# Optimization experiments

Hardware: AMD Instinct MI355X
Metric: run time of the kernel (lower is better)

Reference implementation:

```python
import jax, jax.numpy as jnp
import numpy as np

B, N = 2048, 64
D, H = 64, 256
CARD_V, UNIT_V, ENEMY_V, AT_V, SRC_V, MODE_V, TER_V, SITE_V, SKILL_V = 400, 100, 120, 50, 30, 10, 12, 25, 60
STATE_SC, CE_SC, SITE_SC, ME_SC, ACT_SC = 64, 8, 6, 8, 16
L_HAND, L_UNIT, L_CE, L_SK, L_VS, L_ME, L_TGT = 16, 8, 8, 8, 16, 16, 8
STATE_IN = STATE_SC + 6 * D + (D + CE_SC) + (D + SITE_SC) + (D + ME_SC)  # 662
ACT_IN = 7 * D + ACT_SC  # 464


def setup_inputs() -> dict:
    key = jax.random.key(0)
    ks = iter(jax.random.split(key, 64))
    nrm = lambda shape, s=1.0: jax.random.normal(next(ks), shape, jnp.float32) * s
    ri = lambda shape, hi: jax.random.randint(next(ks), shape, 0, hi, jnp.int32)
    return {
        'state_scalars': nrm((B, STATE_SC)),
        'mode_id': ri((B,), MODE_V), 'terrain_id': ri((B,), TER_V), 'site_type_id': ri((B,), SITE_V),
        'hand_ids': ri((B, L_HAND), CARD_V), 'hand_mask': ri((B, L_HAND), 2),
        'unit_ids': ri((B, L_UNIT), UNIT_V), 'unit_mask': ri((B, L_UNIT), 2),
        'combat_enemy_ids': ri((B, L_CE), ENEMY_V), 'combat_enemy_scalars': nrm((B, L_CE, CE_SC)), 'combat_enemy_mask': ri((B, L_CE), 2),
        'skill_ids': ri((B, L_SK), SKILL_V), 'skill_mask': ri((B, L_SK), 2),
        'visible_site_ids': ri((B, L_VS), SITE_V), 'visible_site_scalars': nrm((B, L_VS, SITE_SC)), 'visible_site_mask': ri((B, L_VS), 2),
        'map_enemy_ids': ri((B, L_ME), ENEMY_V), 'map_enemy_scalars': nrm((B, L_ME, ME_SC)), 'map_enemy_mask': ri((B, L_ME), 2),
        'action_ids': ri((B, N, 6), SRC_V),  # SRC_V=30 is min over the 6 id vocabs -> always in range
        'action_scalars': nrm((B, N, ACT_SC)),
        'target_enemy_ids': ri((B, N, L_TGT), ENEMY_V), 'target_mask': ri((B, N, L_TGT), 2),
        'card_emb': nrm((CARD_V, D), 0.05), 'unit_emb': nrm((UNIT_V, D), 0.05), 'enemy_emb': nrm((ENEMY_V, D), 0.05),
        'action_type_emb': nrm((AT_V, D), 0.05), 'source_emb': nrm((SRC_V, D), 0.05), 'mode_emb': nrm((MODE_V, D), 0.05),
        'terrain_emb': nrm((TER_V, D), 0.05), 'site_emb': nrm((SITE_V, D), 0.05), 'skill_emb': nrm((SKILL_V, D), 0.05),
        'map_site_emb': nrm((SITE_V, D), 0.05),
        'W_s': nrm((STATE_IN, H), 0.02), 'b_s': jnp.zeros((H,), jnp.float32),
        'W_a': nrm((ACT_IN, H), 0.02), 'b_a': jnp.zeros((H,), jnp.float32),
        'W1': nrm((2 * H, H), 0.02), 'b1': jnp.zeros((H,), jnp.float32),
        'W2': nrm((H, 1), 0.02), 'b2': jnp.zeros((1,), jnp.float32),
        'W_v': nrm((H, 1), 0.02), 'b_v': jnp.zeros((1,), jnp.float32),
    }


def masked_mean(x, mask):
    # x: [..., L, D'], mask: [..., L] (0/1). Empty list -> zeros (count clamped to 1).
    m = mask.astype(x.dtype)[..., None]
    s = jnp.sum(x * m, axis=-2)
    c = jnp.maximum(jnp.sum(m, axis=-2), 1.0)
    return s / c


def reference(state_scalars, mode_id, terrain_id, site_type_id, hand_ids, hand_mask,
              unit_ids, unit_mask, combat_enemy_ids, combat_enemy_scalars, combat_enemy_mask,
              skill_ids, skill_mask, visible_site_ids, visible_site_scalars, visible_site_mask,
              map_enemy_ids, map_enemy_scalars, map_enemy_mask, action_ids, action_scalars,
              target_enemy_ids, target_mask, card_emb, unit_emb, enemy_emb, action_type_emb,
              source_emb, mode_emb, terrain_emb, site_emb, skill_emb, map_site_emb,
              W_s, b_s, W_a, b_a, W1, b1, W2, b2, W_v, b_v):
    # ---- state encoding (batched version of encode_state) ----
    hand_pool = masked_mean(card_emb[hand_ids], hand_mask)            # [B, D]
    unit_pool = masked_mean(unit_emb[unit_ids], unit_mask)            # [B, D]
    ce = jnp.concatenate([enemy_emb[combat_enemy_ids], combat_enemy_scalars], axis=-1)
    ce_pool = masked_mean(ce, combat_enemy_mask)                      # [B, D+CE_SC]
    skill_pool = masked_mean(skill_emb[skill_ids], skill_mask)        # [B, D]
    vs = jnp.concatenate([map_site_emb[visible_site_ids], visible_site_scalars], axis=-1)
    vs_pool = masked_mean(vs, visible_site_mask)                      # [B, D+SITE_SC]
    me = jnp.concatenate([enemy_emb[map_enemy_ids], map_enemy_scalars], axis=-1)
    me_pool = masked_mean(me, map_enemy_mask)                         # [B, D+ME_SC]
    state_input = jnp.concatenate([
        state_scalars, mode_emb[mode_id], hand_pool, unit_pool,
        terrain_emb[terrain_id], site_emb[site_type_id],
        ce_pool, skill_pool, vs_pool, me_pool], axis=-1)              # [B, 662]
    state_repr = jnp.tanh(state_input @ W_s + b_s)                    # [B, H]
    # ---- action encoding (batched encode_actions) ----
    tgt_pool = masked_mean(enemy_emb[target_enemy_ids], target_mask)  # [B, N, D]
    action_input = jnp.concatenate([
        action_type_emb[action_ids[..., 0]], source_emb[action_ids[..., 1]],
        card_emb[action_ids[..., 2]], unit_emb[action_ids[..., 3]],
        enemy_emb[action_ids[..., 4]], skill_emb[action_ids[..., 5]],
        tgt_pool, action_scalars], axis=-1)                           # [B, N, 464]
    action_reprs = jnp.tanh(action_input @ W_a + b_a)                 # [B, N, H]
    # ---- scoring + value heads ----
    state_b = jnp.broadcast_to(state_repr[:, None, :], (state_repr.shape[0], action_reprs.shape[1], state_repr.shape[1]))
    combined = jnp.concatenate([state_b, action_reprs], axis=-1)      # [B, N, 2H]
    logits = (jnp.tanh(combined @ W1 + b1) @ W2 + b2)[..., 0]         # [B, N]
    value = (state_repr @ W_v + b_v)[..., 0]                          # [B]
    return logits, value
```

## Files before the change

### kernel.cpp

```cpp
#include <hip/hip_runtime.h>
#include <hip/hip_bf16.h>

#define BB 2048
#define NN 64
#define DD 64
#define HH 256
#define L_HAND 16
#define L_UNIT 8
#define L_CE 8
#define L_SK 8
#define L_VS 16
#define L_ME 16
#define L_TGT 8
#define STATE_SC 64
#define CE_SC 8
#define SITE_SC 6
#define ME_SC 8
#define ACT_SC 16
#define STATE_IN 662
#define ACT_IN 464

#define SROWS 4
#define SK 672
#define SSTRIDE 676

typedef __attribute__((ext_vector_type(8))) short short8;
typedef __attribute__((ext_vector_type(4))) float f32x4;

__device__ __forceinline__ float fast_tanh(float x) {
    float e = __expf(2.0f * x);
    return 1.0f - 2.0f / (e + 1.0f);
}
__device__ __forceinline__ short f2bs(float x) {
    __hip_bfloat16 h = __float2bfloat16(x);
    return *reinterpret_cast<short*>(&h);
}
__device__ __forceinline__ float bs2f(short u) {
    union { unsigned int i; float f; } v;
    v.i = ((unsigned int)(unsigned short)u) << 16;
    return v.f;
}

#define RO_AT    0
#define RO_SRC   50
#define RO_CARD  80
#define RO_UNIT  480
#define RO_ENEMY 580
#define RO_SKILL 700
#define EMB_ROWS 760

#define T0 (480 * 256)
#define T1 (T0 + 256 * 256)
#define T2 (T1 + EMB_ROWS * 64)
#define T3 (T2 + SK * 256)
#define T4 (T3 + 256 * 256)

__global__ __launch_bounds__(256) void pack_kernel(
    const float* __restrict__ W_a, const float* __restrict__ W1,
    const float* __restrict__ W_s,
    const float* __restrict__ at_emb, const float* __restrict__ src_emb,
    const float* __restrict__ card_emb, const float* __restrict__ unit_emb,
    const float* __restrict__ enemy_emb, const float* __restrict__ skill_emb,
    ushort* __restrict__ WaP, ushort* __restrict__ W1bP, ushort* __restrict__ emb16,
    ushort* __restrict__ WsP, ushort* __restrict__ W1aP)
{
    const int idx = blockIdx.x * 256 + threadIdx.x;
    if (idx < T0) {
        const int k = idx >> 8, n = idx & 255;
        const float v = (k < ACT_IN) ? W_a[k * HH + n] : 0.f;
        const int pi = (((k >> 5) * 16 + (n >> 4)) * 64 +
                        ((n & 15) + 16 * ((k >> 3) & 3))) * 8 + (k & 7);
        WaP[pi] = (ushort)f2bs(v);
    } else if (idx < T1) {
        const int j = idx - T0;
        const int k = j >> 8, n = j & 255;
        const float v = W1[(256 + k) * HH + n];
        const int pi = (((k >> 5) * 16 + (n >> 4)) * 64 +
                        ((n & 15) + 16 * ((k >> 3) & 3))) * 8 + (k & 7);
        W1bP[pi] = (ushort)f2bs(v);
    } else if (idx < T2) {
        const int j = idx - T1;
        const int row = j >> 6, d = j & 63;
        float v;
        if      (row < RO_SRC)   v = at_emb[row * 64 + d];
        else if (row < RO_CARD)  v = src_emb[(row - RO_SRC) * 64 + d];
        else if (row < RO_UNIT)  v = card_emb[(row - RO_CARD) * 64 + d];
        else if (row < RO_ENEMY) v = unit_emb[(row - RO_UNIT) * 64 + d];
        else if (row < RO_SKILL) v = enemy_emb[(row - RO_ENEMY) * 64 + d];
        else                     v = skill_emb[(row - RO_SKILL) * 64 + d];
        emb16[j] = (ushort)f2bs(v);
    } else if (idx < T3) {
        const int j = idx - T2;
        const int k = j >> 8, n = j & 255;
        const float v = (k < STATE_IN) ? W_s[k * HH + n] : 0.f;
        const int pi = (((k >> 5) * 16 + (n >> 4)) * 64 +
                        ((n & 15) + 16 * ((k >> 3) & 3))) * 8 + (k & 7);
        WsP[pi] = (ushort)f2bs(v);
    } else if (idx < T4) {
        const int j = idx - T3;
        const int k = j >> 8, n = j & 255;
        const float v = W1[k * HH + n];
        const int pi = (((k >> 5) * 16 + (n >> 4)) * 64 +
                        ((n & 15) + 16 * ((k >> 3) & 3))) * 8 + (k & 7);
        W1aP[pi] = (ushort)f2bs(v);
    }
}

__global__ __launch_bounds__(256) void state_mfma_kernel(
    const float* __restrict__ state_scalars,
    const int* __restrict__ mode_id, const int* __restrict__ terrain_id,
    const int* __restrict__ site_type_id,
    const int* __restrict__ hand_ids, const int* __restrict__ hand_mask,
    const int* __restrict__ unit_ids, const int* __restrict__ unit_mask,
    const int* __restrict__ ce_ids, const float* __restrict__ ce_sc, const int* __restrict__ ce_mask,
    const int* __restrict__ skill_ids, const int* __restrict__ skill_mask,
    const int* __restrict__ vs_ids, const float* __restrict__ vs_sc, const int* __restrict__ vs_mask,
    const int* __restrict__ me_ids, const float* __restrict__ me_sc, const int* __restrict__ me_mask,
    const float* __restrict__ mode_emb, const float* __restrict__ ter_emb,
    const float* __restrict__ site_emb, const float* __restrict__ msite_emb,
    const ushort* __restrict__ emb16,
    const ushort* __restrict__ WsP, const float* __restrict__ b_s,
    const ushort* __restrict__ W1aP,
    const float* __restrict__ W_v, const float* __restrict__ b_v,
    float* __restrict__ s_part, float* __restrict__ out_value)
{
    __shared__ float s_in[SROWS * SSTRIDE];
    __shared__ ushort sA2[8 * 64 * 8];
    __shared__ float red[4][4];

    const int t = threadIdx.x;
    const int b0 = blockIdx.x * SROWS;
    const int w = t >> 6;
    const int lane = t & 63;
    const ushort* card16  = emb16 + RO_CARD  * 64;
    const ushort* unit16  = emb16 + RO_UNIT  * 64;
    const ushort* enemy16 = emb16 + RO_ENEMY * 64;
    const ushort* skill16 = emb16 + RO_SKILL * 64;

    for (int u = t; u < SROWS * 84; u += 256) {
        const int r  = u / 84;
        const int un = u - r * 84;
        const int b  = b0 + r;
        float* dst = s_in + r * SSTRIDE;
        if (un < 8) {
            const int o0 = un * 8;
            const float4 f0 = *(const float4*)(state_scalars + b * STATE_SC + o0);
            const float4 f1 = *(const float4*)(state_scalars + b * STATE_SC + o0 + 4);
            *(float4*)(dst + o0) = f0; *(float4*)(dst + o0 + 4) = f1;
        } else if (un < 16) {
            const int d0 = (un - 8) * 8;
            const float4 f0 = *(const float4*)(mode_emb + mode_id[b] * DD + d0);
            const float4 f1 = *(const float4*)(mode_emb + mode_id[b] * DD + d0 + 4);
            *(float4*)(dst + 64 + d0) = f0; *(float4*)(dst + 64 + d0 + 4) = f1;
        } else if (un < 24) {
            const int d0 = (un - 16) * 8;
            float acc[8] = {0,0,0,0,0,0,0,0}; int c = 0;
#pragma unroll
            for (int l = 0; l < L_HAND; ++l) {
                const int mk = hand_mask[b * L_HAND + l]; c += mk;
                const float fm = (float)mk;
                const short8 e = *(const short8*)(card16 + hand_ids[b * L_HAND + l] * 64 + d0);
#pragma unroll
                for (int q = 0; q < 8; ++q) acc[q] = fmaf(fm, bs2f(e[q]), acc[q]);
            }
            const float inv = 1.0f / (float)(c > 1 ? c : 1);
#pragma unroll
            for (int q = 0; q < 8; ++q) dst[128 + d0 + q] = acc[q] * inv;
        } else if (un < 32) {
            const int d0 = (un - 24) * 8;
            float acc[8] = {0,0,0,0,0,0,0,0}; int c = 0;
#pragma unroll
            for (int l = 0; l < L_UNIT; ++l) {
                const int mk = unit_mask[b * L_UNIT + l]; c += mk;
                const float fm = (float)mk;
                const short8 e = *(const short8*)(unit16 + unit_ids[b * L_UNIT + l] * 64 + d0);
#pragma unroll
                for (int q = 0; q < 8; ++q) acc[q] = fmaf(fm, bs2f(e[q]), acc[q]);
            }
            const float inv = 1.0f / (float)(c > 1 ? c : 1);
#pragma unroll
            for (int q = 0; q < 8; ++q) dst[192 + d0 + q] = acc[q] * inv;
        } else if (un < 40) {
            const int d0 = (un - 32) * 8;
            const float4 f0 = *(const float4*)(ter_emb + terrain_id[b] * DD + d0);
            const float4 f1 = *(const float4*)(ter_emb + terrain_id[b] * DD + d0 + 4);
            *(float4*)(dst + 256 + d0) = f0; *(float4*)(dst + 256 + d0 + 4) = f1;
        } else if (un < 48) {
            const int d0 = (un - 40) * 8;
            const float4 f0 = *(const float4*)(site_emb + site_type_id[b] * DD + d0);
            const float4 f1 = *(const float4*)(site_emb + site_type_id[b] * DD + d0 + 4);
            *(float4*)(dst + 320 + d0) = f0; *(float4*)(dst + 320 + d0 + 4) = f1;
        } else if (un < 56) {
            const int d0 = (un - 48) * 8;
            float acc[8] = {0,0,0,0,0,0,0,0}; int c = 0;
#pragma unroll
            for (int l = 0; l < L_CE; ++l) {
                const int mk = ce_mask[b * L_CE + l]; c += mk;
                const float fm = (float)mk;
                const short8 e = *(const short8*)(enemy16 + ce_ids[b * L_CE + l] * 64 + d0);
#pragma unroll
                for (int q = 0; q < 8; ++q) acc[q] = fmaf(fm, bs2f(e[q]), acc[q]);
            }
            const float inv = 1.0f / (float)(c > 1 ? c : 1);
#pragma unroll
            for (int q = 0; q < 8; ++q) dst[384 + d0 + q] = acc[q] * inv;
        } else if (un == 56) {
            float acc[8] = {0,0,0,0,0,0,0,0}; int c = 0;
#pragma unroll
            for (int l = 0; l < L_CE; ++l) {
                const int mk = ce_mask[b * L_CE + l]; c += mk;
                const float fm = (float)mk;
                const float4 f0 = *(const float4*)(ce_sc + (b * L_CE + l) * CE_SC);
                const float4 f1 = *(const float4*)(ce_sc + (b * L_CE + l) * CE_SC + 4);
                acc[0] = fmaf(fm, f0.x, acc[0]); acc[1] = fmaf(fm, f0.y, acc[1]);
                acc[2] = fmaf(fm, f0.z, acc[2]); acc[3] = fmaf(fm, f0.w, acc[3]);
                acc[4] = fmaf(fm, f1.x, acc[4]); acc[5] = fmaf(fm, f1.y, acc[5]);
                acc[6] = fmaf(fm, f1.z, acc[6]); acc[7] = fmaf(fm, f1.w, acc[7]);
            }
            const float inv = 1.0f / (float)(c > 1 ? c : 1);
#pragma unroll
            for (int q = 0; q < 8; ++q) dst[448 + q] = acc[q] * inv;
        } else if (un < 65) {
            const int d0 = (un - 57) * 8;
            float acc[8] = {0,0,0,0,0,0,0,0}; int c = 0;
#pragma unroll
            for (int l = 0; l < L_SK; ++l) {
                const int mk = skill_mask[b * L_SK + l]; c += mk;
                const float fm = (float)mk;
                const short8 e = *(const short8*)(skill16 + skill_ids[b * L_SK + l] * 64 + d0);
#pragma unroll
                for (int q = 0; q < 8; ++q) acc[q] = fmaf(fm, bs2f(e[q]), acc[q]);
            }
            const float inv = 1.0f / (float)(c > 1 ? c : 1);
#pragma unroll
            for (int q = 0; q < 8; ++q) dst[456 + d0 + q] = acc[q] * inv;
        } else if (un < 73) {
            const int d0 = (un - 65) * 8;
            float acc[8] = {0,0,0,0,0,0,0,0}; int c = 0;
#pragma unroll
            for (int l = 0; l < L_VS; ++l) {
                const int mk = vs_mask[b * L_VS + l]; c += mk;
                const float fm = (float)mk;
                const float4 f0 = *(const float4*)(msite_emb + vs_ids[b * L_VS + l] * DD + d0);
                const float4 f1 = *(const float4*)(msite_emb + vs_ids[b * L_VS + l] * DD + d0 + 4);
                acc[0] = fmaf(fm, f0.x, acc[0]); acc[1] = fmaf(fm, f0.y, acc[1]);
                acc[2] = fmaf(fm, f0.z, acc[2]); acc[3] = fmaf(fm, f0.w, acc[3]);
                acc[4] = fmaf(fm, f1.x, acc[4]); acc[5] = fmaf(fm, f1.y, acc[5]);
                acc[6] = fmaf(fm, f1.z, acc[6]); acc[7] = fmaf(fm, f1.w, acc[7]);
            }
            const float inv = 1.0f / (float)(c > 1 ? c : 1);
#pragma unroll
            for (int q = 0; q < 8; ++q) dst[520 + d0 + q] = acc[q] * inv;
        } else if (un == 73) {
            float acc[6] = {0,0,0,0,0,0}; int c = 0;
#pragma unroll
            for (int l = 0; l < L_VS; ++l) {
                const int mk = vs_mask[b * L_VS + l]; c += mk;
                const float fm = (float)mk;
                const float* p = vs_sc + (b * L_VS + l) * SITE_SC;
#pragma unroll
                for (int q = 0; q < 6; ++q) acc[q] = fmaf(fm, p[q], acc[q]);
            }
            const float inv = 1.0f / (float)(c > 1 ? c : 1);
#pragma unroll
            for (int q = 0; q < 6; ++q) dst[584 + q] = acc[q] * inv;
        } else if (un < 82) {
            const int d0 = (un - 74) * 8;
            float acc[8] = {0,0,0,0,0,0,0,0}; int c = 0;
#pragma unroll
            for (int l = 0; l < L_ME; ++l) {
                const int mk = me_mask[b * L_ME + l]; c += mk;
                const float fm = (float)mk;
                const short8 e = *(const short8*)(enemy16 + me_ids[b * L_ME + l] * 64 + d0);
#pragma unroll
                for (int q = 0; q < 8; ++q) acc[q] = fmaf(fm, bs2f(e[q]), acc[q]);
            }
            const float inv = 1.0f / (float)(c > 1 ? c : 1);
#pragma unroll
            for (int q = 0; q < 8; ++q) dst[590 + d0 + q] = acc[q] * inv;
        } else if (un == 82) {
            float acc[8] = {0,0,0,0,0,0,0,0}; int c = 0;
#pragma unroll
            for (int l = 0; l < L_ME; ++l) {
                const int mk = me_mask[b * L_ME + l]; c += mk;
                const float fm = (float)mk;
                const float4 f0 = *(const float4*)(me_sc + (b * L_ME + l) * ME_SC);
                const float4 f1 = *(const float4*)(me_sc + (b * L_ME + l) * ME_SC + 4);
                acc[0] = fmaf(fm, f0.x, acc[0]); acc[1] = fmaf(fm, f0.y, acc[1]);
                acc[2] = fmaf(fm, f0.z, acc[2]); acc[3] = fmaf(fm, f0.w, acc[3]);
                acc[4] = fmaf(fm, f1.x, acc[4]); acc[5] = fmaf(fm, f1.y, acc[5]);
                acc[6] = fmaf(fm, f1.z, acc[6]); acc[7] = fmaf(fm, f1.w, acc[7]);
            }
            const float inv = 1.0f / (float)(c > 1 ? c : 1);
#pragma unroll
            for (int q = 0; q < 8; ++q) dst[654 + q] = acc[q] * inv;
        } else {
#pragma unroll
            for (int q = 0; q < 10; ++q) dst[662 + q] = 0.f;
        }
    }
    __syncthreads();

    const short8* Ws8  = (const short8*)WsP;
    const short8* W1a8 = (const short8*)W1aP;
    const f32x4 zero = {0.f, 0.f, 0.f, 0.f};
    const int m15 = lane & 15;
    const int g = lane >> 4;
    const float* arow = s_in + (m15 & 3) * SSTRIDE;

    f32x4 acc1[4];
#pragma unroll
    for (int nt = 0; nt < 4; ++nt) acc1[nt] = zero;

    for (int kt = 0; kt < 21; ++kt) {
        const int k0 = kt * 32 + 8 * g;
        const float4 v0 = *(const float4*)(arow + k0);
        const float4 v1 = *(const float4*)(arow + k0 + 4);
        short8 a;
        a[0] = f2bs(v0.x); a[1] = f2bs(v0.y); a[2] = f2bs(v0.z); a[3] = f2bs(v0.w);
        a[4] = f2bs(v1.x); a[5] = f2bs(v1.y); a[6] = f2bs(v1.z); a[7] = f2bs(v1.w);
        short8 bfr[4];
#pragma unroll
        for (int nt = 0; nt < 4; ++nt) bfr[nt] = Ws8[(kt * 16 + w * 4 + nt) * 64 + lane];
#pragma unroll
        for (int nt = 0; nt < 4; ++nt)
            acc1[nt] = __builtin_amdgcn_mfma_f32_16x16x32_bf16(a, bfr[nt], acc1[nt], 0, 0, 0);
    }

    float sr[4][4];
    float pv[4] = {0.f, 0.f, 0.f, 0.f};
#pragma unroll
    for (int nt = 0; nt < 4; ++nt) {
        const int n = w * 64 + nt * 16 + m15;
        const float bsn = b_s[n];
        const float wvn = W_v[n];
#pragma unroll
        for (int r = 0; r < 4; ++r) {
            const float sv = fast_tanh(acc1[nt][r] + bsn);
            sr[nt][r] = sv;
            pv[r] = fmaf(sv, wvn, pv[r]);
        }
    }
#pragma unroll
    for (int r = 0; r < 4; ++r) {
        float v = pv[r];
        v += __shfl_xor(v, 1);
        v += __shfl_xor(v, 2);
        v += __shfl_xor(v, 4);
        v += __shfl_xor(v, 8);
        if (lane == 0) red[w][r] = v;
    }
    if (g == 0) {
#pragma unroll
        for (int nt = 0; nt < 4; ++nt) {
            const int n = w * 64 + nt * 16 + m15;
            const int kt2 = n >> 5;
            const int lo16 = (n >> 3) & 3;
#pragma unroll
            for (int r = 0; r < 4; ++r) {
                const int pi = (kt2 * 64 + (r + 16 * lo16)) * 8 + (n & 7);
                sA2[pi] = (ushort)f2bs(sr[nt][r]);
            }
        }
    }
    __syncthreads();

    if (t < SROWS) {
        out_value[b0 + t] = red[0][t] + red[1][t] + red[2][t] + red[3][t] + b_v[0];
    }

    const short8* sA2_8 = (const short8*)sA2;
    f32x4 acc2[4];
#pragma unroll
    for (int nt = 0; nt < 4; ++nt) acc2[nt] = zero;
#pragma unroll
    for (int kt = 0; kt < 8; ++kt) {
        const short8 a2 = sA2_8[kt * 64 + lane];
        short8 bfr[4];
#pragma unroll
        for (int nt = 0; nt < 4; ++nt) bfr[nt] = W1a8[(kt * 16 + w * 4 + nt) * 64 + lane];
#pragma unroll
        for (int nt = 0; nt < 4; ++nt)
            acc2[nt] = __builtin_amdgcn_mfma_f32_16x16x32_bf16(a2, bfr[nt], acc2[nt], 0, 0, 0);
    }
    if (g == 0) {
#pragma unroll
        for (int nt = 0; nt < 4; ++nt) {
            const int n = w * 64 + nt * 16 + m15;
#pragma unroll
            for (int r = 0; r < 4; ++r)
                s_part[(b0 + r) * HH + n] = acc2[nt][r];
        }
    }
}

__device__ __forceinline__ short8 build_chunk(
    int kc, int m, int b,
    const int* __restrict__ s_ids, const int* __restrict__ s_tid,
    const int* __restrict__ s_tmk, const ushort* __restrict__ emb16,
    const float* __restrict__ action_scalars)
{
    const int k0 = kc << 3;
    short8 val;
    if (k0 < 384) {
        const int j = k0 >> 6;
        int roff;
        if      (j == 0) roff = RO_AT;
        else if (j == 1) roff = RO_SRC;
        else if (j == 2) roff = RO_CARD;
        else if (j == 3) roff = RO_UNIT;
        else if (j == 4) roff = RO_ENEMY;
        else             roff = RO_SKILL;
        const int id = s_ids[m * 6 + j];
        val = *(const short8*)(emb16 + (roff + id) * 64 + (k0 & 63));
    } else if (k0 < 448) {
        const int d = k0 - 384;
        const ushort* enemy16 = emb16 + RO_ENEMY * 64;
        float accq[8] = {0.f, 0.f, 0.f, 0.f, 0.f, 0.f, 0.f, 0.f};
        int c = 0;
#pragma unroll
        for (int l = 0; l < L_TGT; ++l) {
            const int mk = s_tmk[m * 8 + l];
            c += mk;
            const float fm = (float)mk;
            const short8 e = *(const short8*)(enemy16 + s_tid[m * 8 + l] * 64 + d);
#pragma unroll
            for (int q = 0; q < 8; ++q) accq[q] = fmaf(fm, bs2f(e[q]), accq[q]);
        }
        const float inv = 1.0f / (float)(c > 1 ? c : 1);
#pragma unroll
        for (int q = 0; q < 8; ++q) val[q] = f2bs(accq[q] * inv);
    } else if (k0 < 464) {
        const float* sc = action_scalars + (b * NN + m) * ACT_SC + (k0 - 448);
        const float4 f0 = *(const float4*)sc;
        const float4 f1 = *(const float4*)(sc + 4);
        val[0] = f2bs(f0.x); val[1] = f2bs(f0.y); val[2] = f2bs(f0.z); val[3] = f2bs(f0.w);
        val[4] = f2bs(f1.x); val[5] = f2bs(f1.y); val[6] = f2bs(f1.z); val[7] = f2bs(f1.w);
    } else {
#pragma unroll
        for (int q = 0; q < 8; ++q) val[q] = 0;
    }
    return val;
}

__global__ __launch_bounds__(512) void action_mfma_kernel(
    const int* __restrict__ action_ids, const float* __restrict__ action_scalars,
    const int* __restrict__ tgt_ids, const int* __restrict__ tgt_mask,
    const ushort* __restrict__ emb16,
    const ushort* __restrict__ WaP, const float* __restrict__ b_a,
    const ushort* __restrict__ W1bP, const float* __restrict__ b1,
    const float* __restrict__ W2, const float* __restrict__ b2,
    const float* __restrict__ s_part, float* __restrict__ out_logits)
{
    __shared__ ushort sA[8 * 4 * 64 * 8];
    __shared__ float red[8][64];
    __shared__ int s_ids[64 * 6];
    __shared__ int s_tid[64 * 8];
    __shared__ int s_tmk[64 * 8];

    const int t = threadIdx.x;
    const int b = blockIdx.x;
    const int w = t >> 6;
    const int lane = t & 63;

    for (int i = t; i < 64 * 6; i += 512) s_ids[i] = action_ids[b * (64 * 6) + i];
    for (int i = t; i < 64 * 8; i += 512) {
        s_tid[i] = tgt_ids[b * (64 * 8) + i];
        s_tmk[i] = tgt_mask[b * (64 * 8) + i];
    }
    __syncthreads();

    const short8* sA8  = (const short8*)sA;
    short8* sA8w = (short8*)sA;
    const short8* Wa8  = (const short8*)WaP;
    const short8* W1b8 = (const short8*)W1bP;
    const f32x4 zero = {0.f, 0.f, 0.f, 0.f};
    const int m15 = lane & 15;
    const int m = lane;
    const int mt_b = m >> 4, mrow = m & 15;

    for (int kc = w; kc < 32; kc += 8) {
        const short8 val = build_chunk(kc, m, b, s_ids, s_tid, s_tmk, emb16, action_scalars);
        const int kt = kc >> 2, lo = kc & 3;
        sA8w[(kt * 4 + mt_b) * 64 + mrow + 16 * lo] = val;
    }
    __syncthreads();

    float ba[2];
#pragma unroll
    for (int nt = 0; nt < 2; ++nt) ba[nt] = b_a[w * 32 + nt * 16 + m15];

    f32x4 acc[4][2];
#pragma unroll
    for (int i = 0; i < 4; ++i) { acc[i][0] = zero; acc[i][1] = zero; }

    short8 bn0 = Wa8[(w * 2 + 0) * 64 + lane];
    short8 bn1 = Wa8[(w * 2 + 1) * 64 + lane];
#pragma unroll
    for (int kt = 0; kt < 8; ++kt) {
        const short8 b0 = bn0, b1 = bn1;
        bn0 = Wa8[((kt + 1) * 16 + w * 2 + 0) * 64 + lane];
        bn1 = Wa8[((kt + 1) * 16 + w * 2 + 1) * 64 + lane];
        short8 a[4];
#pragma unroll
        for (int mti = 0; mti < 4; ++mti) a[mti] = sA8[(kt * 4 + mti) * 64 + lane];
#pragma unroll
        for (int mti = 0; mti < 4; ++mti) {
            acc[mti][0] = __builtin_amdgcn_mfma_f32_16x16x32_bf16(a[mti], b0, acc[mti][0], 0, 0, 0);
            acc[mti][1] = __builtin_amdgcn_mfma_f32_16x16x32_bf16(a[mti], b1, acc[mti][1], 0, 0, 0);
        }
    }
    __syncthreads();

    for (int kc = 32 + w; kc < 60; kc += 8) {
        const short8 val = build_chunk(kc, m, b, s_ids, s_tid, s_tmk, emb16, action_scalars);
        const int ktl = (kc >> 2) - 8, lo = kc & 3;
        sA8w[(ktl * 4 + mt_b) * 64 + mrow + 16 * lo] = val;
    }
    __syncthreads();

#pragma unroll
    for (int kt = 8; kt < 15; ++kt) {
        const short8 b0 = bn0, b1 = bn1;
        if (kt < 14) {
            bn0 = Wa8[((kt + 1) * 16 + w * 2 + 0) * 64 + lane];
            bn1 = Wa8[((kt + 1) * 16 + w * 2 + 1) * 64 + lane];
        }
        short8 a[4];
#pragma unroll
        for (int mti = 0; mti < 4; ++mti) a[mti] = sA8[((kt - 8) * 4 + mti) * 64 + lane];
#pragma unroll
        for (int mti = 0; mti < 4; ++mti) {
            acc[mti][0] = __builtin_amdgcn_mfma_f32_16x16x32_bf16(a[mti], b0, acc[mti][0], 0, 0, 0);
            acc[mti][1] = __builtin_amdgcn_mfma_f32_16x16x32_bf16(a[mti], b1, acc[mti][1], 0, 0, 0);
        }
    }
    __syncthreads();

    short8 cn0 = W1b8[(w * 2 + 0) * 64 + lane];
    short8 cn1 = W1b8[(w * 2 + 1) * 64 + lane];

#pragma unroll
    for (int mti = 0; mti < 4; ++mti)
#pragma unroll
        for (int nt = 0; nt < 2; ++nt) {
            const int n = w * 32 + nt * 16 + m15;
            const int kt2 = n >> 5;
            const int lo16 = (n >> 3) & 3;
#pragma unroll
            for (int r = 0; r < 4; ++r) {
                const int mm = mti * 16 + (lane >> 4) * 4 + r;
                const float h = fast_tanh(acc[mti][nt][r] + ba[nt]);
                const int pi = ((kt2 * 4 + mti) * 64 + ((mm & 15) + 16 * lo16)) * 8 + (n & 7);
                sA[pi] = (ushort)f2bs(h);
            }
        }
    __syncthreads();

    float sp[2], w2v[2];
#pragma unroll
    for (int nt = 0; nt < 2; ++nt) {
        const int n = w * 32 + nt * 16 + m15;
        sp[nt]  = s_part[b * HH + n] + b1[n];
        w2v[nt] = W2[n];
    }

#pragma unroll
    for (int i = 0; i < 4; ++i) { acc[i][0] = zero; acc[i][1] = zero; }

#pragma unroll
    for (int kt = 0; kt < 8; ++kt) {
        const short8 b0 = cn0, b1 = cn1;
        if (kt < 7) {
            cn0 = W1b8[((kt + 1) * 16 + w * 2 + 0) * 64 + lane];
            cn1 = W1b8[((kt + 1) * 16 + w * 2 + 1) * 64 + lane];
        }
        short8 a[4];
#pragma unroll
        for (int mti = 0; mti < 4; ++mti) a[mti] = sA8[(kt * 4 + mti) * 64 + lane];
#pragma unroll
        for (int mti = 0; mti < 4; ++mti) {
            acc[mti][0] = __builtin_amdgcn_mfma_f32_16x16x32_bf16(a[mti], b0, acc[mti][0], 0, 0, 0);
            acc[mti][1] = __builtin_amdgcn_mfma_f32_16x16x32_bf16(a[mti], b1, acc[mti][1], 0, 0, 0);
        }
    }

    float part[4][4];
#pragma unroll
    for (int mti = 0; mti < 4; ++mti)
#pragma unroll
        for (int r = 0; r < 4; ++r) part[mti][r] = 0.f;

#pragma unroll
    for (int mti = 0; mti < 4; ++mti)
#pragma unroll
        for (int nt = 0; nt < 2; ++nt)
#pragma unroll
            for (int r = 0; r < 4; ++r)
                part[mti][r] += fast_tanh(acc[mti][nt][r] + sp[nt]) * w2v[nt];

#pragma unroll
    for (int mti = 0; mti < 4; ++mti)
#pragma unroll
        for (int r = 0; r < 4; ++r) {
            float v = part[mti][r];
            v += __shfl_xor(v, 1);
            v += __shfl_xor(v, 2);
            v += __shfl_xor(v, 4);
            v += __shfl_xor(v, 8);
            part[mti][r] = v;
        }
    if (m15 == 0) {
#pragma unroll
        for (int mti = 0; mti < 4; ++mti)
#pragma unroll
            for (int r = 0; r < 4; ++r) {
                const int mm = mti * 16 + (lane >> 4) * 4 + r;
                red[w][mm] = part[mti][r];
            }
    }
    __syncthreads();
    if (t < 64) {
        float s = b2[0];
#pragma unroll
        for (int wi = 0; wi < 8; ++wi) s += red[wi][t];
        out_logits[b * NN + t] = s;
    }
}

extern "C" void kernel_launch(void* const* d_in, const int* in_sizes, int n_in,
                              void* d_out, int out_size, void* d_ws, size_t ws_size,
                              hipStream_t stream) {
    const float* state_scalars = (const float*)d_in[0];
    const int*   mode_id       = (const int*)d_in[1];
    const int*   terrain_id    = (const int*)d_in[2];
    const int*   site_type_id  = (const int*)d_in[3];
    const int*   hand_ids      = (const int*)d_in[4];
    const int*   hand_mask     = (const int*)d_in[5];
    const int*   unit_ids      = (const int*)d_in[6];
    const int*   unit_mask     = (const int*)d_in[7];
    const int*   ce_ids        = (const int*)d_in[8];
    const float* ce_sc         = (const float*)d_in[9];
    const int*   ce_mask       = (const int*)d_in[10];
    const int*   skill_ids     = (const int*)d_in[11];
    const int*   skill_mask    = (const int*)d_in[12];
    const int*   vs_ids        = (const int*)d_in[13];
    const float* vs_sc         = (const float*)d_in[14];
    const int*   vs_mask       = (const int*)d_in[15];
    const int*   me_ids        = (const int*)d_in[16];
    const float* me_sc         = (const float*)d_in[17];
    const int*   me_mask       = (const int*)d_in[18];
    const int*   action_ids    = (const int*)d_in[19];
    const float* action_scalars= (const float*)d_in[20];
    const int*   tgt_ids       = (const int*)d_in[21];
    const int*   tgt_mask      = (const int*)d_in[22];
    const float* card_emb      = (const float*)d_in[23];
    const float* unit_emb      = (const float*)d_in[24];
    const float* enemy_emb     = (const float*)d_in[25];
    const float* at_emb        = (const float*)d_in[26];
    const float* src_emb       = (const float*)d_in[27];
    const float* mode_emb      = (const float*)d_in[28];
    const float* ter_emb       = (const float*)d_in[29];
    const float* site_emb      = (const float*)d_in[30];
    const float* skill_emb     = (const float*)d_in[31];
    const float* msite_emb     = (const float*)d_in[32];
    const float* W_s           = (const float*)d_in[33];
    const float* b_s           = (const float*)d_in[34];
    const float* W_a           = (const float*)d_in[35];
    const float* b_a           = (const float*)d_in[36];
    const float* W1            = (const float*)d_in[37];
    const float* b1            = (const float*)d_in[38];
    const float* W2            = (const float*)d_in[39];
    const float* b2            = (const float*)d_in[40];
    const float* W_v           = (const float*)d_in[41];
    const float* b_v           = (const float*)d_in[42];

    float* out_logits = (float*)d_out;
    float* out_value  = (float*)d_out + (size_t)BB * NN;

    char* ws = (char*)d_ws;
    float*  s_part = (float*)ws;
    ushort* WaP    = (ushort*)(ws + 2097152);
    ushort* W1bP   = (ushort*)(ws + 2342912);
    ushort* emb16  = (ushort*)(ws + 2473984);
    ushort* WsP    = (ushort*)(ws + 2571264);
    ushort* W1aP   = (ushort*)(ws + 2915328);

    pack_kernel<<<(T4 + 255) / 256, 256, 0, stream>>>(
        W_a, W1, W_s, at_emb, src_emb, card_emb, unit_emb, enemy_emb, skill_emb,
        WaP, W1bP, emb16, WsP, W1aP);

    state_mfma_kernel<<<BB / SROWS, 256, 0, stream>>>(
        state_scalars, mode_id, terrain_id, site_type_id,
        hand_ids, hand_mask, unit_ids, unit_mask,
        ce_ids, ce_sc, ce_mask, skill_ids, skill_mask,
        vs_ids, vs_sc, vs_mask, me_ids, me_sc, me_mask,
        mode_emb, ter_emb, site_emb, msite_emb, emb16,
        WsP, b_s, W1aP, W_v, b_v, s_part, out_value);

    action_mfma_kernel<<<BB, 512, 0, stream>>>(
        action_ids, action_scalars, tgt_ids, tgt_mask,
        emb16, WaP, b_a, W1bP, b1, W2, b2, s_part, out_logits);
}
```

Baseline: 123.7 us.

## Stream embedding gathers into LDS asynchronously and reorder action GEMM k-tiles

Embedding-row gathers for the action input now go straight from global memory into LDS via global_load_lds. The tail (target pooling and scalars) is built first, and the GEMM k-loop is reordered (0-7, then 12-14, then 8-11) so the second batch of async gathers overlaps with MFMA work. The change also swaps the tanh division for a hardware reciprocal and replaces the shuffle-xor reduction with DPP row shifts. The aim is to hide gather latency and cut register round trips. The trade-offs are a larger LDS footprint, and correctness now relies on async-copy completion ordering at the barriers.

```diff
diff --git a/kernel.cpp b/kernel.cpp
--- a/kernel.cpp
+++ b/kernel.cpp
@@ -29,7 +29,7 @@
 
 __device__ __forceinline__ float fast_tanh(float x) {
     float e = __expf(2.0f * x);
-    return 1.0f - 2.0f / (e + 1.0f);
+    return 1.0f - 2.0f * __builtin_amdgcn_rcpf(e + 1.0f);
 }
 __device__ __forceinline__ short f2bs(float x) {
     __hip_bfloat16 h = __float2bfloat16(x);
@@ -39,6 +39,23 @@
     union { unsigned int i; float f; } v;
     v.i = ((unsigned int)(unsigned short)u) << 16;
     return v.f;
+}
+__device__ __forceinline__ void async_copy16(const void* gsrc, void* ldst) {
+    __builtin_amdgcn_global_load_lds(
+        (const __attribute__((address_space(1))) unsigned int*)gsrc,
+        (__attribute__((address_space(3))) unsigned int*)ldst, 16, 0, 0);
+}
+__device__ __forceinline__ float sum16_dpp(float v) {
+    int x;
+    x = __builtin_amdgcn_update_dpp(0, __float_as_int(v), 0x111, 0xf, 0xf, true);
+    v += __int_as_float(x);
+    x = __builtin_amdgcn_update_dpp(0, __float_as_int(v), 0x112, 0xf, 0xf, true);
+    v += __int_as_float(x);
+    x = __builtin_amdgcn_update_dpp(0, __float_as_int(v), 0x114, 0xf, 0xf, true);
+    v += __int_as_float(x);
+    x = __builtin_amdgcn_update_dpp(0, __float_as_int(v), 0x118, 0xf, 0xf, true);
+    v += __int_as_float(x);
+    return v;
 }
 
 #define RO_AT    0
@@ -394,26 +411,13 @@
     }
 }
 
-__device__ __forceinline__ short8 build_chunk(
-    int kc, int m, int b,
-    const int* __restrict__ s_ids, const int* __restrict__ s_tid,
-    const int* __restrict__ s_tmk, const ushort* __restrict__ emb16,
-    const float* __restrict__ action_scalars)
+__device__ __forceinline__ short8 tail_chunk(
+    int k0, int m, int b,
+    const int* __restrict__ s_tid, const int* __restrict__ s_tmk,
+    const ushort* __restrict__ emb16, const float* __restrict__ action_scalars)
 {
-    const int k0 = kc << 3;
     short8 val;
-    if (k0 < 384) {
-        const int j = k0 >> 6;
-        int roff;
-        if      (j == 0) roff = RO_AT;
-        else if (j == 1) roff = RO_SRC;
-        else if (j == 2) roff = RO_CARD;
-        else if (j == 3) roff = RO_UNIT;
-        else if (j == 4) roff = RO_ENEMY;
-        else             roff = RO_SKILL;
-        const int id = s_ids[m * 6 + j];
-        val = *(const short8*)(emb16 + (roff + id) * 64 + (k0 & 63));
-    } else if (k0 < 448) {
+    if (k0 < 448) {
         const int d = k0 - 384;
         const ushort* enemy16 = emb16 + RO_ENEMY * 64;
         float accq[8] = {0.f, 0.f, 0.f, 0.f, 0.f, 0.f, 0.f, 0.f};
@@ -452,7 +456,7 @@
     const float* __restrict__ W2, const float* __restrict__ b2,
     const float* __restrict__ s_part, float* __restrict__ out_logits)
 {
-    __shared__ ushort sA[8 * 4 * 64 * 8];
+    __shared__ ushort sA[11 * 2048];
     __shared__ float red[8][64];
     __shared__ int s_ids[64 * 6];
     __shared__ int s_tid[64 * 8];
@@ -462,45 +466,66 @@
     const int b = blockIdx.x;
     const int w = t >> 6;
     const int lane = t & 63;
-
-    for (int i = t; i < 64 * 6; i += 512) s_ids[i] = action_ids[b * (64 * 6) + i];
-    for (int i = t; i < 64 * 8; i += 512) {
-        s_tid[i] = tgt_ids[b * (64 * 8) + i];
-        s_tmk[i] = tgt_mask[b * (64 * 8) + i];
-    }
-    __syncthreads();
+    const int m15 = lane & 15;
 
     const short8* sA8  = (const short8*)sA;
     short8* sA8w = (short8*)sA;
     const short8* Wa8  = (const short8*)WaP;
     const short8* W1b8 = (const short8*)W1bP;
     const f32x4 zero = {0.f, 0.f, 0.f, 0.f};
-    const int m15 = lane & 15;
-    const int m = lane;
-    const int mt_b = m >> 4, mrow = m & 15;
-
-    for (int kc = w; kc < 32; kc += 8) {
-        const short8 val = build_chunk(kc, m, b, s_ids, s_tid, s_tmk, emb16, action_scalars);
-        const int kt = kc >> 2, lo = kc & 3;
-        sA8w[(kt * 4 + mt_b) * 64 + mrow + 16 * lo] = val;
-    }
-    __syncthreads();
-
-    float ba[2];
-#pragma unroll
-    for (int nt = 0; nt < 2; ++nt) ba[nt] = b_a[w * 32 + nt * 16 + m15];
-
-    f32x4 acc[4][2];
-#pragma unroll
-    for (int i = 0; i < 4; ++i) { acc[i][0] = zero; acc[i][1] = zero; }
 
     short8 bn0 = Wa8[(w * 2 + 0) * 64 + lane];
     short8 bn1 = Wa8[(w * 2 + 1) * 64 + lane];
+
+    for (int i = t; i < 64 * 6; i += 512) s_ids[i] = action_ids[b * (64 * 6) + i];
+    for (int i = t; i < 64 * 8; i += 512) {
+        s_tid[i] = tgt_ids[b * (64 * 8) + i];
+        s_tmk[i] = tgt_mask[b * (64 * 8) + i];
+    }
+    __syncthreads();
+
+    const int ROFFS[6] = {RO_AT, RO_SRC, RO_CARD, RO_UNIT, RO_ENEMY, RO_SKILL};
+
+    {
+        const int kt = w;
+        const int j = kt >> 1;
+        const int roff = ROFFS[j];
+        const int koff = (kt & 1) * 32 + (lane >> 4) * 8;
+#pragma unroll
+        for (int i = 0; i < 4; ++i) {
+            const int id = s_ids[(i * 16 + m15) * 6 + j];
+            const ushort* src = emb16 + (roff + id) * 64 + koff;
+            async_copy16(src, sA + kt * 2048 + i * 512);
+        }
+    }
+
+    {
+        const int m = lane;
+        const int mt_b = m >> 4, mrow = m & 15;
+        for (int kc = 48 + w; kc < 60; kc += 8) {
+            const int k0 = kc << 3;
+            const short8 val = tail_chunk(k0, m, b, s_tid, s_tmk, emb16, action_scalars);
+            const int ktl = (k0 >> 5) - 4;
+            const int lo = kc & 3;
+            sA8w[(ktl * 4 + mt_b) * 64 + mrow + 16 * lo] = val;
+        }
+    }
+    __syncthreads();
+
+    float ba[2];
+#pragma unroll
+    for (int nt = 0; nt < 2; ++nt) ba[nt] = b_a[w * 32 + nt * 16 + m15];
+
+    f32x4 acc[4][2];
+#pragma unroll
+    for (int i = 0; i < 4; ++i) { acc[i][0] = zero; acc[i][1] = zero; }
+
 #pragma unroll
     for (int kt = 0; kt < 8; ++kt) {
         const short8 b0 = bn0, b1 = bn1;
-        bn0 = Wa8[((kt + 1) * 16 + w * 2 + 0) * 64 + lane];
-        bn1 = Wa8[((kt + 1) * 16 + w * 2 + 1) * 64 + lane];
+        const int nkt = (kt < 7) ? kt + 1 : 12;
+        bn0 = Wa8[(nkt * 16 + w * 2 + 0) * 64 + lane];
+        bn1 = Wa8[(nkt * 16 + w * 2 + 1) * 64 + lane];
         short8 a[4];
 #pragma unroll
         for (int mti = 0; mti < 4; ++mti) a[mti] = sA8[(kt * 4 + mti) * 64 + lane];
@@ -512,23 +537,28 @@
     }
     __syncthreads();
 
-    for (int kc = 32 + w; kc < 60; kc += 8) {
-        const short8 val = build_chunk(kc, m, b, s_ids, s_tid, s_tmk, emb16, action_scalars);
-        const int ktl = (kc >> 2) - 8, lo = kc & 3;
-        sA8w[(ktl * 4 + mt_b) * 64 + mrow + 16 * lo] = val;
-    }
-    __syncthreads();
-
-#pragma unroll
-    for (int kt = 8; kt < 15; ++kt) {
+    if (w < 4) {
+        const int kt = 8 + w;
+        const int j = kt >> 1;
+        const int roff = ROFFS[j];
+        const int koff = (kt & 1) * 32 + (lane >> 4) * 8;
+#pragma unroll
+        for (int i = 0; i < 4; ++i) {
+            const int id = s_ids[(i * 16 + m15) * 6 + j];
+            const ushort* src = emb16 + (roff + id) * 64 + koff;
+            async_copy16(src, sA + (kt - 8) * 2048 + i * 512);
+        }
+    }
+
+#pragma unroll
+    for (int kt = 12; kt < 15; ++kt) {
         const short8 b0 = bn0, b1 = bn1;
-        if (kt < 14) {
-            bn0 = Wa8[((kt + 1) * 16 + w * 2 + 0) * 64 + lane];
-            bn1 = Wa8[((kt + 1) * 16 + w * 2 + 1) * 64 + lane];
-        }
+        const int nkt = (kt < 14) ? kt + 1 : 8;
+        bn0 = Wa8[(nkt * 16 + w * 2 + 0) * 64 + lane];
+        bn1 = Wa8[(nkt * 16 + w * 2 + 1) * 64 + lane];
         short8 a[4];
 #pragma unroll
-        for (int mti = 0; mti < 4; ++mti) a[mti] = sA8[((kt - 8) * 4 + mti) * 64 + lane];
+        for (int mti = 0; mti < 4; ++mti) a[mti] = sA8[((kt - 4) * 4 + mti) * 64 + lane];
 #pragma unroll
         for (int mti = 0; mti < 4; ++mti) {
             acc[mti][0] = __builtin_amdgcn_mfma_f32_16x16x32_bf16(a[mti], b0, acc[mti][0], 0, 0, 0);
@@ -537,8 +567,27 @@
     }
     __syncthreads();
 
-    short8 cn0 = W1b8[(w * 2 + 0) * 64 + lane];
-    short8 cn1 = W1b8[(w * 2 + 1) * 64 + lane];
+    short8 cn0, cn1;
+#pragma unroll
+    for (int kt = 8; kt < 12; ++kt) {
+        const short8 b0 = bn0, b1 = bn1;
+        if (kt < 11) {
+            bn0 = Wa8[((kt + 1) * 16 + w * 2 + 0) * 64 + lane];
+            bn1 = Wa8[((kt + 1) * 16 + w * 2 + 1) * 64 + lane];
+        } else {
+            cn0 = W1b8[(w * 2 + 0) * 64 + lane];
+            cn1 = W1b8[(w * 2 + 1) * 64 + lane];
+        }
+        short8 a[4];
+#pragma unroll
+        for (int mti = 0; mti < 4; ++mti) a[mti] = sA8[((kt - 8) * 4 + mti) * 64 + lane];
+#pragma unroll
+        for (int mti = 0; mti < 4; ++mti) {
+            acc[mti][0] = __builtin_amdgcn_mfma_f32_16x16x32_bf16(a[mti], b0, acc[mti][0], 0, 0, 0);
+            acc[mti][1] = __builtin_amdgcn_mfma_f32_16x16x32_bf16(a[mti], b1, acc[mti][1], 0, 0, 0);
+        }
+    }
+    __syncthreads();
 
 #pragma unroll
     for (int mti = 0; mti < 4; ++mti)
@@ -602,15 +651,10 @@
 #pragma unroll
     for (int mti = 0; mti < 4; ++mti)
 #pragma unroll
-        for (int r = 0; r < 4; ++r) {
-            float v = part[mti][r];
-            v += __shfl_xor(v, 1);
-            v += __shfl_xor(v, 2);
-            v += __shfl_xor(v, 4);
-            v += __shfl_xor(v, 8);
-            part[mti][r] = v;
-        }
-    if (m15 == 0) {
+        for (int r = 0; r < 4; ++r)
+            part[mti][r] = sum16_dpp(part[mti][r]);
+
+    if (m15 == 15) {
 #pragma unroll
         for (int mti = 0; mti < 4; ++mti)
 #pragma unroll
```

Result: faster. 112.3 us (-9.2%).
